# Performance work log

Hardware: AMD Instinct MI355X
Metric: run time of the kernel (lower is better)

## Reference

```python
import jax, jax.numpy as jnp
import numpy as np

D = 1024
H = 16
HD = D // H


def setup_inputs() -> dict:
    key = jax.random.key(0)
    ks = jax.random.split(key, 13)
    s = 0.02
    inp = {
        "x": jax.random.normal(ks[0], (2, 2048, D), dtype=jnp.float32),
        "Wq": jax.random.normal(ks[1], (D, D), dtype=jnp.float32) * s,
        "bq": jnp.zeros((D,), jnp.float32),
        "Wk": jax.random.normal(ks[2], (D, D), dtype=jnp.float32) * s,
        "bk": jnp.zeros((D,), jnp.float32),
        "Wv": jax.random.normal(ks[3], (D, D), dtype=jnp.float32) * s,
        "bv": jnp.zeros((D,), jnp.float32),
        "Wo": jax.random.normal(ks[4], (D, D), dtype=jnp.float32) * s,
        "bo": jnp.zeros((D,), jnp.float32),
        "W1": jax.random.normal(ks[5], (D, 4 * D), dtype=jnp.float32) * s,
        "b1": jnp.zeros((4 * D,), jnp.float32),
        "W2": jax.random.normal(ks[6], (4 * D, D), dtype=jnp.float32) * s,
        "b2": jnp.zeros((D,), jnp.float32),
    }
    return inp


def reference(x, Wq, bq, Wk, bk, Wv, bv, Wo, bo, W1, b1, W2, b2):
    B, L, _ = x.shape
    # attention (dropout = identity in eval); note: original forward never applies norm1/norm2
    q = (x @ Wq + bq).reshape(B, L, H, HD).transpose(0, 2, 1, 3)  # [B,H,L,HD]
    k = (x @ Wk + bk).reshape(B, L, H, HD).transpose(0, 2, 1, 3)
    v = (x @ Wv + bv).reshape(B, L, H, HD).transpose(0, 2, 1, 3)
    s = jnp.einsum("bhqd,bhkd->bhqk", q, k) / jnp.sqrt(jnp.float32(HD))
    causal = jnp.tril(jnp.ones((L, L), dtype=bool))
    s = jnp.where(causal[None, None, :, :], s, -jnp.inf)
    p = jax.nn.softmax(s, axis=-1)
    y = jnp.einsum("bhqk,bhkd->bhqd", p, v)
    y = y.transpose(0, 2, 1, 3).reshape(B, L, D)
    x = x + (y @ Wo + bo)
    # MLP with SiLU
    h = jax.nn.silu(x @ W1 + b1)
    x = x + (h @ W2 + b2)
    return x
```

## Files before the change

### kernel.cpp

```cpp
#include <hip/hip_runtime.h>
#include <hip/hip_bf16.h>
#include <stdint.h>

using u16 = unsigned short;
typedef __bf16 bf16x8 __attribute__((ext_vector_type(8)));
typedef float f32x4 __attribute__((ext_vector_type(4)));
typedef u16 u16x8 __attribute__((ext_vector_type(8)));

__device__ __forceinline__ float bf2f(u16 u) {
  union { unsigned int i; float f; } v; v.i = ((unsigned int)u) << 16; return v.f;
}
__device__ __forceinline__ u16 f2bf(float f) {
  __bf16 h = (__bf16)f;
  return __builtin_bit_cast(u16, h);
}
__device__ __forceinline__ float fexp2(float x) {
  return __builtin_amdgcn_exp2f(x);
}

__device__ __forceinline__ void gload_lds16(const void* g, void* l) {
  __builtin_amdgcn_global_load_lds(
      (__attribute__((address_space(1))) const void*)g,
      (__attribute__((address_space(3))) void*)l, 16, 0, 0);
}

__global__ void cvt_f32_bf16(const float* __restrict__ in, u16* __restrict__ out) {
  int i = (blockIdx.x * 256 + threadIdx.x) * 8;
  float4 a = *(const float4*)(in + i);
  float4 b = *(const float4*)(in + i + 4);
  u16x8 o;
  o[0] = f2bf(a.x); o[1] = f2bf(a.y); o[2] = f2bf(a.z); o[3] = f2bf(a.w);
  o[4] = f2bf(b.x); o[5] = f2bf(b.y); o[6] = f2bf(b.z); o[7] = f2bf(b.w);
  *(u16x8*)(out + i) = o;
}

__global__ void transpose_cvt(const float* __restrict__ W, u16* __restrict__ Wt,
                              int K, int N) {
  __shared__ float t[32][33];
  const int tx = threadIdx.x & 31, ty = threadIdx.x >> 5;
  const int n0 = blockIdx.x * 32, k0 = blockIdx.y * 32;
#pragma unroll
  for (int i = 0; i < 32; i += 8)
    t[ty + i][tx] = W[(size_t)(k0 + ty + i) * N + n0 + tx];
  __syncthreads();
#pragma unroll
  for (int i = 0; i < 32; i += 8)
    Wt[(size_t)(n0 + ty + i) * K + k0 + tx] = f2bf(t[tx][ty + i]);
}

__global__ void transpose_cvt4(const float* __restrict__ Wa, const float* __restrict__ Wb,
                               const float* __restrict__ Wc, const float* __restrict__ Wd,
                               u16* __restrict__ Da, u16* __restrict__ Db,
                               u16* __restrict__ Dc, u16* __restrict__ Dd) {
  __shared__ float t[32][33];
  const int z = blockIdx.z;
  const float* W = (z == 0) ? Wa : (z == 1) ? Wb : (z == 2) ? Wc : Wd;
  u16* D = (z == 0) ? Da : (z == 1) ? Db : (z == 2) ? Dc : Dd;
  const int tx = threadIdx.x & 31, ty = threadIdx.x >> 5;
  const int n0 = blockIdx.x * 32, k0 = blockIdx.y * 32;
#pragma unroll
  for (int i = 0; i < 32; i += 8)
    t[ty + i][tx] = W[(size_t)(k0 + ty + i) * 1024 + n0 + tx];
  __syncthreads();
#pragma unroll
  for (int i = 0; i < 32; i += 8)
    D[(size_t)(n0 + ty + i) * 1024 + k0 + tx] = f2bf(t[tx][ty + i]);
}

__global__ void transpose_v(const u16* __restrict__ qkv, u16* __restrict__ vt) {
  __shared__ u16 tile[32][34];
  const int tx = threadIdx.x & 31, ty = threadIdx.x >> 5;
  const int kv0 = blockIdx.x * 32, d0 = blockIdx.y * 32;
  const int bh = blockIdx.z, b = bh >> 4, h = bh & 15;
#pragma unroll
  for (int i = 0; i < 32; i += 8)
    tile[ty + i][tx] = qkv[(size_t)(b * 2048 + kv0 + ty + i) * 3072 + 2048 + h * 64 + d0 + tx];
  __syncthreads();
#pragma unroll
  for (int i = 0; i < 32; i += 8)
    vt[((size_t)bh * 64 + d0 + ty + i) * 2048 + kv0 + tx] = tile[tx][ty + i];
}

__global__ void concat_bias(const float* __restrict__ bq, const float* __restrict__ bk,
                            const float* __restrict__ bv, float* __restrict__ o) {
  int i = blockIdx.x * 256 + threadIdx.x;
  o[i] = (i < 1024) ? bq[i] : (i < 2048 ? bk[i - 1024] : bv[i - 2048]);
}

template <int EPI>
__global__ __launch_bounds__(512, 2) void gemm256_kernel(
    const u16* __restrict__ A, const u16* __restrict__ Bt,
    const float* __restrict__ bias, u16* __restrict__ outb,
    int M, int N, int K) {
  __shared__ u16 As[4][8192];
  __shared__ u16 Bs[4][8192];
  const int t = threadIdx.x;
  const int w = t >> 6, lane = t & 63, lr = lane & 15, lg = lane >> 4;
  const int wm = w >> 2, wn = w & 3;
  const int gx = gridDim.x;
  const int nwg = gx * gridDim.y;
  const int p = blockIdx.y * gx + blockIdx.x;
  const int L = (p & 7) * (nwg >> 3) + (p >> 3);
  const int m0 = (L / gx) * 256, n0 = (L % gx) * 256;

  f32x4 acc[8][4] = {};
  bf16x8 bfr[4];
  const int NKT = K >> 5;

  auto stageA = [&](int kt) {
#pragma unroll
    for (int l = 0; l < 2; ++l) {
      int slot = l * 512 + t;
      int row = slot >> 2, cs = slot & 3;
      int ss = cs ^ ((row >> 1) & 3);
      gload_lds16(&A[(size_t)(m0 + row) * K + kt * 32 + ss * 8], &As[kt & 3][slot * 8]);
    }
  };
  auto stageB = [&](int kt) {
#pragma unroll
    for (int l = 0; l < 2; ++l) {
      int slot = l * 512 + t;
      int row = slot >> 2, cs = slot & 3;
      int ss = cs ^ ((row >> 1) & 3);
      gload_lds16(&Bt[(size_t)(n0 + row) * K + kt * 32 + ss * 8], &Bs[kt & 3][slot * 8]);
    }
  };

  stageA(0); stageB(0); stageA(1); stageB(1); stageA(2); stageB(2);
  asm volatile("s_waitcnt vmcnt(8)" ::: "memory");
  __builtin_amdgcn_s_barrier();

#define PHASE(Q, STAGE)                                                          \
  {                                                                              \
    const u16* Ab = &As[kt & 3][0];                                              \
    bf16x8 af[4];                                                                \
    _Pragma("unroll") for (int m = 0; m < 4; ++m) {                              \
      int row = wm * 128 + ((Q) * 4 + m) * 16 + lr;                              \
      int sl = lg ^ ((row >> 1) & 3);                                            \
      af[m] = *(const bf16x8*)&Ab[row * 32 + sl * 8];                            \
    }                                                                            \
    if ((Q) == 0) {                                                              \
      const u16* Bb = &Bs[kt & 3][0];                                            \
      _Pragma("unroll") for (int n = 0; n < 4; ++n) {                            \
        int row = wn * 64 + n * 16 + lr;                                         \
        int sl = lg ^ ((row >> 1) & 3);                                          \
        bfr[n] = *(const bf16x8*)&Bb[row * 32 + sl * 8];                         \
      }                                                                          \
    }                                                                            \
    STAGE;                                                                       \
    __builtin_amdgcn_s_barrier();                                                \
    asm volatile("s_waitcnt lgkmcnt(0)" ::: "memory");                           \
    __builtin_amdgcn_sched_barrier(0);                                           \
    __builtin_amdgcn_s_setprio(1);                                               \
    _Pragma("unroll") for (int m = 0; m < 4; ++m)                                \
        _Pragma("unroll") for (int n = 0; n < 4; ++n)                            \
            acc[(Q) * 4 + m][n] = __builtin_amdgcn_mfma_f32_16x16x32_bf16(       \
                af[m], bfr[n], acc[(Q) * 4 + m][n], 0, 0, 0);                    \
    __builtin_amdgcn_s_setprio(0);                                               \
  }

  int kt = 0;
  for (; kt < NKT - 3; ++kt) {
    PHASE(0, stageA(kt + 3));
    __builtin_amdgcn_s_barrier();
    PHASE(1, stageB(kt + 3));
    asm volatile("s_waitcnt vmcnt(8)" ::: "memory");
    __builtin_amdgcn_s_barrier();
  }
  asm volatile("s_waitcnt vmcnt(0)" ::: "memory");
  __builtin_amdgcn_s_barrier();
  for (; kt < NKT; ++kt) {
    PHASE(0, (void)0);
    __builtin_amdgcn_s_barrier();
    PHASE(1, (void)0);
    __builtin_amdgcn_s_barrier();
  }
#undef PHASE

#pragma unroll
  for (int mf = 0; mf < 8; ++mf)
#pragma unroll
    for (int nf = 0; nf < 4; ++nf)
#pragma unroll
      for (int i = 0; i < 4; ++i) {
        int gr = m0 + wm * 128 + mf * 16 + lg * 4 + i;
        int gc = n0 + wn * 64 + nf * 16 + lr;
        float v = acc[mf][nf][i] + bias[gc];
        if constexpr (EPI == 1) v = v / (1.f + __expf(-v));
        outb[(size_t)gr * N + gc] = f2bf(v);
      }
}

template <int EPI>
__global__ __launch_bounds__(256) void gemm_nk64_kernel(
    const u16* __restrict__ A, const u16* __restrict__ Bt,
    const float* __restrict__ bias, const float* __restrict__ resid,
    u16* __restrict__ outb, float* __restrict__ outf, int M, int N, int K) {
  __shared__ u16 As[2][128 * 64];
  __shared__ u16 Bs[2][64 * 64];
  const int t = threadIdx.x;
  const int w = t >> 6, lane = t & 63, lr = lane & 15, lg = lane >> 4;
  const int wm = w >> 1, wn = w & 1;
  const int gx = gridDim.x;
  const int nwg = gx * gridDim.y;
  const int p = blockIdx.y * gx + blockIdx.x;
  const int L = (p & 7) * (nwg >> 3) + (p >> 3);
  const int m0 = (L / gx) * 128, n0 = (L % gx) * 64;

  f32x4 acc[4][2] = {};
  const int nt = K >> 6;

  auto stage = [&](int kt, int buf) {
#pragma unroll
    for (int it = 0; it < 4; ++it) {
      int ofs = (it * 256 + t) * 8;
      int row = ofs >> 6, slot = (ofs >> 3) & 7, ss = slot ^ (row & 7);
      gload_lds16(&A[(size_t)(m0 + row) * K + kt * 64 + ss * 8], &As[buf][ofs]);
    }
#pragma unroll
    for (int it = 0; it < 2; ++it) {
      int ofs = (it * 256 + t) * 8;
      int row = ofs >> 6, slot = (ofs >> 3) & 7, ss = slot ^ (row & 7);
      gload_lds16(&Bt[(size_t)(n0 + row) * K + kt * 64 + ss * 8], &Bs[buf][ofs]);
    }
  };

  stage(0, 0);
  __syncthreads();

  for (int kt = 0; kt < nt; ++kt) {
    const int cur = kt & 1;
    if (kt + 1 < nt) stage(kt + 1, cur ^ 1);
#pragma unroll
    for (int kk = 0; kk < 64; kk += 32) {
      const int kcol = kk + lg * 8;
      bf16x8 af[4], bfr[2];
#pragma unroll
      for (int m = 0; m < 4; ++m) {
        int row = wm * 64 + m * 16 + lr;
        int ss = (kcol >> 3) ^ (row & 7);
        af[m] = *(const bf16x8*)&As[cur][row * 64 + ss * 8];
      }
#pragma unroll
      for (int n = 0; n < 2; ++n) {
        int row = wn * 32 + n * 16 + lr;
        int ss = (kcol >> 3) ^ (row & 7);
        bfr[n] = *(const bf16x8*)&Bs[cur][row * 64 + ss * 8];
      }
#pragma unroll
      for (int m = 0; m < 4; ++m)
#pragma unroll
        for (int n = 0; n < 2; ++n)
          acc[m][n] = __builtin_amdgcn_mfma_f32_16x16x32_bf16(af[m], bfr[n],
                                                              acc[m][n], 0, 0, 0);
    }
    __syncthreads();
  }

  const int r0 = m0 + wm * 64, c0 = n0 + wn * 32;
#pragma unroll
  for (int m = 0; m < 4; ++m)
#pragma unroll
    for (int n = 0; n < 2; ++n)
#pragma unroll
      for (int i = 0; i < 4; ++i) {
        int gr = r0 + m * 16 + lg * 4 + i;
        int gc = c0 + n * 16 + lr;
        float v = acc[m][n][i] + bias[gc];
        if constexpr (EPI == 2 || EPI == 3) v += resid[(size_t)gr * N + gc];
        if constexpr (EPI == 2) {
          outf[(size_t)gr * N + gc] = v;
          outb[(size_t)gr * N + gc] = f2bf(v);
        }
        if constexpr (EPI == 3) outf[(size_t)gr * N + gc] = v;
      }
}

__global__ __launch_bounds__(512) void attn_kernel(const u16* __restrict__ qkv,
                                                   const u16* __restrict__ vtg,
                                                   u16* __restrict__ out) {
  __shared__ u16 smem[24576];
  const int t = threadIdx.x, w = t >> 6, lane = t & 63, lr = lane & 15, lg = lane >> 4;
  const int p = blockIdx.y * 16 + blockIdx.x;
  const int L = (p & 7) * 64 + (p >> 3);
  const int qt = 15 - (L & 15), bh = L >> 4, b = bh >> 4, h = bh & 15;
  const int qbw = qt * 128 + w * 16;
  const int jmax_blk = 2 * qt + 1;
  const int jmax_w = 2 * qt + (w >> 2);

  const float QS = 0.18033688011f;
  bf16x8 qf[2];
#pragma unroll
  for (int kc = 0; kc < 2; ++kc) {
    const u16x8 v = *(const u16x8*)&qkv[(size_t)(b * 2048 + qbw + lr) * 3072 +
                                        h * 64 + kc * 32 + lg * 8];
    bf16x8 q;
#pragma unroll
    for (int jj = 0; jj < 8; ++jj) q[jj] = (__bf16)(bf2f(v[jj]) * QS);
    qf[kc] = q;
  }

  f32x4 yacc[4] = {};
  float S = 0.f;

  auto stage = [&](int j, int buf) {
    u16* Kb = smem + buf * 4096;
    u16* Vb = smem + 8192 + buf * 4096;
    int ofs = t * 8;
    int row = ofs >> 6, slot = (ofs >> 3) & 7, ss = slot ^ (row & 7);
    gload_lds16(&qkv[(size_t)(b * 2048 + j * 64 + row) * 3072 + 1024 + h * 64 + ss * 8],
                &Kb[ofs]);
    gload_lds16(&vtg[((size_t)bh * 64 + row) * 2048 + j * 64 + ss * 8],
                &Vb[ofs]);
  };

  stage(0, 0);
  __syncthreads();

  for (int j = 0; j <= jmax_blk; ++j) {
    const int cur = j & 1;
    if (j < jmax_blk) stage(j + 1, cur ^ 1);

    if (j <= jmax_w) {
      const char* Kc = (const char*)(smem + cur * 4096);
      const char* Vc = (const char*)(smem + 8192 + cur * 4096);
      char* Pw = (char*)(smem + 16384 + w * 1024);

      bf16x8 kf[2][4];
#pragma unroll
      for (int kc = 0; kc < 2; ++kc)
#pragma unroll
        for (int n = 0; n < 4; ++n) {
          int row = n * 16 + lr;
          kf[kc][n] = *(const bf16x8*)(Kc + row * 128 +
                                       ((kc * 64 + lg * 16) ^ ((row & 7) << 4)));
        }
      f32x4 s[4] = {};
#pragma unroll
      for (int n = 0; n < 4; ++n)
#pragma unroll
        for (int kc = 0; kc < 2; ++kc)
          s[n] = __builtin_amdgcn_mfma_f32_16x16x32_bf16(kf[kc][n], qf[kc],
                                                         s[n], 0, 0, 0);
      if (j * 64 + 63 > qbw) {
#pragma unroll
        for (int n = 0; n < 4; ++n)
#pragma unroll
          for (int i = 0; i < 4; ++i) {
            int kabs = j * 64 + n * 16 + lg * 4 + i;
            int qabs = qbw + lr;
            if (kabs > qabs) s[n][i] = -1e30f;
          }
      }
      {
        float rs = 0.f;
#pragma unroll
        for (int n = 0; n < 4; ++n)
#pragma unroll
          for (int i = 0; i < 4; ++i) {
            float pv = fexp2(s[n][i]);
            s[n][i] = pv;
            rs += pv;
          }
        S += rs;
        const int qrow = lr, sw = (qrow & 7) << 4;
#pragma unroll
        for (int n = 0; n < 4; ++n) {
          ushort4 ph;
          ph.x = f2bf(s[n][0]); ph.y = f2bf(s[n][1]);
          ph.z = f2bf(s[n][2]); ph.w = f2bf(s[n][3]);
          *(ushort4*)(Pw + qrow * 128 + ((n * 32 + lg * 8) ^ sw)) = ph;
        }
      }
#pragma unroll
      for (int kc = 0; kc < 2; ++kc) {
        bf16x8 pa, vtf[4];
        {
          int qrow = lr;
          pa = *(const bf16x8*)(Pw + qrow * 128 +
                                ((kc * 64 + lg * 16) ^ ((qrow & 7) << 4)));
        }
#pragma unroll
        for (int n = 0; n < 4; ++n) {
          int row = n * 16 + lr;
          vtf[n] = *(const bf16x8*)(Vc + row * 128 +
                                    ((kc * 64 + lg * 16) ^ ((row & 7) << 4)));
        }
#pragma unroll
        for (int n = 0; n < 4; ++n)
          yacc[n] = __builtin_amdgcn_mfma_f32_16x16x32_bf16(pa, vtf[n],
                                                            yacc[n], 0, 0, 0);
      }
    }
    __syncthreads();
  }

  {
    float Sv = S;
    Sv += __shfl_xor(Sv, 16, 64);
    Sv += __shfl_xor(Sv, 32, 64);
    float inv = 1.f / Sv;
#pragma unroll
    for (int i = 0; i < 4; ++i) {
      float ivq = __shfl(inv, lg * 4 + i, 64);
#pragma unroll
      for (int n = 0; n < 4; ++n) {
        int row = b * 2048 + qbw + lg * 4 + i;
        int col = h * 64 + n * 16 + lr;
        out[(size_t)row * 1024 + col] = f2bf(yacc[n][i] * ivq);
      }
    }
  }
}

extern "C" void kernel_launch(void* const* d_in, const int* in_sizes, int n_in,
                              void* d_out, int out_size, void* d_ws, size_t ws_size,
                              hipStream_t stream) {
  const float* x  = (const float*)d_in[0];
  const float* Wq = (const float*)d_in[1];
  const float* bq = (const float*)d_in[2];
  const float* Wk = (const float*)d_in[3];
  const float* bk = (const float*)d_in[4];
  const float* Wv = (const float*)d_in[5];
  const float* bv = (const float*)d_in[6];
  const float* Wo = (const float*)d_in[7];
  const float* bo = (const float*)d_in[8];
  const float* W1 = (const float*)d_in[9];
  const float* b1 = (const float*)d_in[10];
  const float* W2 = (const float*)d_in[11];
  const float* b2 = (const float*)d_in[12];
  float* out = (float*)d_out;

  char* ws = (char*)d_ws;
  const size_t MB = 1u << 20;
  u16*   xb    = (u16*)(ws + 0);
  u16*   wtqkv = (u16*)(ws + 8 * MB);
  u16*   wto   = (u16*)(ws + 14 * MB);
  u16*   wt1   = (u16*)(ws + 16 * MB);
  u16*   wt2   = (u16*)(ws + 24 * MB);
  float* bqkv  = (float*)(ws + 32 * MB);
  u16*   qkv   = (u16*)(ws + 33 * MB);
  u16*   attn  = (u16*)(ws + 57 * MB);
  float* x2f   = (float*)(ws + 65 * MB);
  u16*   x2b   = (u16*)(ws + 81 * MB);
  u16*   hbuf  = (u16*)(ws + 89 * MB);
  u16*   vtg   = xb;

  cvt_f32_bf16<<<2048, 256, 0, stream>>>(x, xb);
  transpose_cvt4<<<dim3(32, 32, 4), 256, 0, stream>>>(
      Wq, Wk, Wv, Wo, wtqkv, wtqkv + 1024 * 1024, wtqkv + 2 * 1024 * 1024, wto);
  transpose_cvt<<<dim3(128, 32), 256, 0, stream>>>(W1, wt1, 1024, 4096);
  transpose_cvt<<<dim3(32, 128), 256, 0, stream>>>(W2, wt2, 4096, 1024);
  concat_bias<<<12, 256, 0, stream>>>(bq, bk, bv, bqkv);

  gemm256_kernel<0><<<dim3(12, 16), 512, 0, stream>>>(
      xb, wtqkv, bqkv, qkv, 4096, 3072, 1024);
  transpose_v<<<dim3(64, 2, 32), 256, 0, stream>>>(qkv, vtg);
  attn_kernel<<<dim3(16, 32), 512, 0, stream>>>(qkv, vtg, attn);
  gemm_nk64_kernel<2><<<dim3(16, 32), 256, 0, stream>>>(
      attn, wto, bo, x, x2b, x2f, 4096, 1024, 1024);
  gemm256_kernel<1><<<dim3(16, 16), 512, 0, stream>>>(
      x2b, wt1, b1, hbuf, 4096, 4096, 1024);
  gemm_nk64_kernel<3><<<dim3(16, 32), 256, 0, stream>>>(
      hbuf, wt2, b2, x2f, nullptr, out, 4096, 1024, 4096);
}
```

Measured before the change: 221.9 us.

## Deepen nk64 GEMM pipeline to four K=32 stages with vmcnt-based waits

Replaces the double-buffered K=64 tile loop in the N=64 GEMM kernel with a four-stage ring of K=32 tiles. Three tiles are kept in flight, and partial s_waitcnt vmcnt plus raw s_barrier are used in place of full __syncthreads. LDS swizzling is adapted to the 32-wide rows, and s_setprio is raised around the MFMA block. The goal is to hide global-load latency better and lower barrier cost, in exchange for more barriers per K and reliance on hand-tuned waitcnt counts that must match the number of loads issued per stage.

Measured after the change: 250.0 us. 1.13x slower.

```diff
diff --git a/kernel.cpp b/kernel.cpp
--- a/kernel.cpp
+++ b/kernel.cpp
@@ -196,8 +196,8 @@
     const u16* __restrict__ A, const u16* __restrict__ Bt,
     const float* __restrict__ bias, const float* __restrict__ resid,
     u16* __restrict__ outb, float* __restrict__ outf, int M, int N, int K) {
-  __shared__ u16 As[2][128 * 64];
-  __shared__ u16 Bs[2][64 * 64];
+  __shared__ u16 As[4][128 * 32];
+  __shared__ u16 Bs[4][64 * 32];
   const int t = threadIdx.x;
   const int w = t >> 6, lane = t & 63, lr = lane & 15, lg = lane >> 4;
   const int wm = w >> 1, wn = w & 1;
@@ -208,54 +208,67 @@
   const int m0 = (L / gx) * 128, n0 = (L % gx) * 64;
 
   f32x4 acc[4][2] = {};
-  const int nt = K >> 6;
-
-  auto stage = [&](int kt, int buf) {
-#pragma unroll
-    for (int it = 0; it < 4; ++it) {
-      int ofs = (it * 256 + t) * 8;
-      int row = ofs >> 6, slot = (ofs >> 3) & 7, ss = slot ^ (row & 7);
-      gload_lds16(&A[(size_t)(m0 + row) * K + kt * 64 + ss * 8], &As[buf][ofs]);
-    }
-#pragma unroll
-    for (int it = 0; it < 2; ++it) {
-      int ofs = (it * 256 + t) * 8;
-      int row = ofs >> 6, slot = (ofs >> 3) & 7, ss = slot ^ (row & 7);
-      gload_lds16(&Bt[(size_t)(n0 + row) * K + kt * 64 + ss * 8], &Bs[buf][ofs]);
+  const int NKT = K >> 5;
+
+  auto stage = [&](int kt) {
+    const int buf = kt & 3;
+#pragma unroll
+    for (int l = 0; l < 2; ++l) {
+      int slot = l * 256 + t;
+      int row = slot >> 2, cs = slot & 3;
+      int ss = cs ^ ((row >> 1) & 3);
+      gload_lds16(&A[(size_t)(m0 + row) * K + kt * 32 + ss * 8], &As[buf][slot * 8]);
+    }
+    {
+      int slot = t;
+      int row = slot >> 2, cs = slot & 3;
+      int ss = cs ^ ((row >> 1) & 3);
+      gload_lds16(&Bt[(size_t)(n0 + row) * K + kt * 32 + ss * 8], &Bs[buf][slot * 8]);
     }
   };
 
-  stage(0, 0);
-  __syncthreads();
-
-  for (int kt = 0; kt < nt; ++kt) {
-    const int cur = kt & 1;
-    if (kt + 1 < nt) stage(kt + 1, cur ^ 1);
-#pragma unroll
-    for (int kk = 0; kk < 64; kk += 32) {
-      const int kcol = kk + lg * 8;
-      bf16x8 af[4], bfr[2];
-#pragma unroll
-      for (int m = 0; m < 4; ++m) {
-        int row = wm * 64 + m * 16 + lr;
-        int ss = (kcol >> 3) ^ (row & 7);
-        af[m] = *(const bf16x8*)&As[cur][row * 64 + ss * 8];
-      }
-#pragma unroll
-      for (int n = 0; n < 2; ++n) {
-        int row = wn * 32 + n * 16 + lr;
-        int ss = (kcol >> 3) ^ (row & 7);
-        bfr[n] = *(const bf16x8*)&Bs[cur][row * 64 + ss * 8];
-      }
-#pragma unroll
-      for (int m = 0; m < 4; ++m)
-#pragma unroll
-        for (int n = 0; n < 2; ++n)
-          acc[m][n] = __builtin_amdgcn_mfma_f32_16x16x32_bf16(af[m], bfr[n],
-                                                              acc[m][n], 0, 0, 0);
-    }
-    __syncthreads();
-  }
+#define NK64_COMP(KT)                                                            \
+  {                                                                              \
+    const u16* Ab = &As[(KT) & 3][0];                                            \
+    const u16* Bb = &Bs[(KT) & 3][0];                                            \
+    bf16x8 af[4], bfr[2];                                                        \
+    _Pragma("unroll") for (int m = 0; m < 4; ++m) {                              \
+      int row = wm * 64 + m * 16 + lr;                                           \
+      int sl = lg ^ ((row >> 1) & 3);                                            \
+      af[m] = *(const bf16x8*)&Ab[row * 32 + sl * 8];                            \
+    }                                                                            \
+    _Pragma("unroll") for (int n = 0; n < 2; ++n) {                              \
+      int row = wn * 32 + n * 16 + lr;                                           \
+      int sl = lg ^ ((row >> 1) & 3);                                            \
+      bfr[n] = *(const bf16x8*)&Bb[row * 32 + sl * 8];                           \
+    }                                                                            \
+    asm volatile("s_waitcnt lgkmcnt(0)" ::: "memory");                           \
+    __builtin_amdgcn_sched_barrier(0);                                           \
+    __builtin_amdgcn_s_setprio(1);                                               \
+    _Pragma("unroll") for (int m = 0; m < 4; ++m)                                \
+        _Pragma("unroll") for (int n = 0; n < 2; ++n)                            \
+          acc[m][n] = __builtin_amdgcn_mfma_f32_16x16x32_bf16(af[m], bfr[n],     \
+                                                              acc[m][n], 0, 0, 0);\
+    __builtin_amdgcn_s_setprio(0);                                               \
+  }
+
+  stage(0); stage(1); stage(2);
+  asm volatile("s_waitcnt vmcnt(6)" ::: "memory");
+  __builtin_amdgcn_s_barrier();
+
+  int kt = 0;
+  for (; kt < NKT - 3; ++kt) {
+    stage(kt + 3);
+    NK64_COMP(kt);
+    asm volatile("s_waitcnt vmcnt(6)" ::: "memory");
+    __builtin_amdgcn_s_barrier();
+  }
+  asm volatile("s_waitcnt vmcnt(0)" ::: "memory");
+  __builtin_amdgcn_s_barrier();
+  for (; kt < NKT; ++kt) {
+    NK64_COMP(kt);
+  }
+#undef NK64_COMP
 
   const int r0 = m0 + wm * 64, c0 = n0 + wn * 32;
 #pragma unroll
```
